# Kernel optimization log

Hardware: AMD Instinct MI355X
Metric: run time of the kernel (lower is better)

Reference implementation:

```python
import jax, jax.numpy as jnp
import numpy as np

EMB = 1024
N_HEADS = 16
HEAD = EMB // N_HEADS
EPS = 1e-5


def layernorm(x, g, b):
    mu = jnp.mean(x, axis=-1, keepdims=True)
    var = jnp.var(x, axis=-1, keepdims=True)
    return (x - mu) * jax.lax.rsqrt(var + EPS) * g + b


def setup_inputs() -> dict:
    key = jax.random.key(0)
    ks = jax.random.split(key, 12)
    s = lambda fan_in: 1.0 / np.sqrt(fan_in)
    return {
        "x": jax.random.normal(ks[0], (8, 1024, EMB), dtype=jnp.float32),
        "ln1_g": jnp.ones((EMB,), jnp.float32),
        "ln1_b": jnp.zeros((EMB,), jnp.float32),
        "wq": jax.random.uniform(ks[1], (EMB, EMB), jnp.float32, -s(EMB), s(EMB)),
        "wk": jax.random.uniform(ks[2], (EMB, EMB), jnp.float32, -s(EMB), s(EMB)),
        "wv": jax.random.uniform(ks[3], (EMB, EMB), jnp.float32, -s(EMB), s(EMB)),
        "w_proj": jax.random.uniform(ks[4], (EMB, EMB), jnp.float32, -s(EMB), s(EMB)),
        "b_proj": jnp.zeros((EMB,), jnp.float32),
        "ln2_g": jnp.ones((EMB,), jnp.float32),
        "ln2_b": jnp.zeros((EMB,), jnp.float32),
        "w1": jax.random.uniform(ks[5], (EMB, 4 * EMB), jnp.float32, -s(EMB), s(EMB)),
        "b1": jnp.zeros((4 * EMB,), jnp.float32),
        "w2": jax.random.uniform(ks[6], (4 * EMB, EMB), jnp.float32, -s(4 * EMB), s(4 * EMB)),
        "b2": jnp.zeros((EMB,), jnp.float32),
    }


def reference(x, ln1_g, ln1_b, wq, wk, wv, w_proj, b_proj, ln2_g, ln2_b, w1, b1, w2, b2):
    B, T, E = x.shape
    h = layernorm(x, ln1_g, ln1_b)
    # per-head no-bias projections == one big matmul then split into heads
    q = (h @ wq).reshape(B, T, N_HEADS, HEAD).transpose(0, 2, 1, 3)  # [B,H,T,D]
    k = (h @ wk).reshape(B, T, N_HEADS, HEAD).transpose(0, 2, 1, 3)
    v = (h @ wv).reshape(B, T, N_HEADS, HEAD).transpose(0, 2, 1, 3)
    scores = jnp.einsum("bhqd,bhkd->bhqk", q, k) * (HEAD ** -0.5)
    causal = jnp.tril(jnp.ones((T, T), dtype=bool))
    scores = jnp.where(causal, scores, -jnp.inf)
    wei = jax.nn.softmax(scores, axis=-1)  # dropout is identity at eval
    attn = jnp.einsum("bhqk,bhkd->bhqd", wei, v)
    attn = attn.transpose(0, 2, 1, 3).reshape(B, T, E)
    out = x + attn @ w_proj + b_proj
    h2 = layernorm(out, ln2_g, ln2_b)
    mlp = jax.nn.gelu(h2 @ w1 + b1, approximate=False) @ w2 + b2
    return out + mlp
```

## Files before the change

### kernel.cpp

```cpp
#include <hip/hip_runtime.h>
#include <hip/hip_bf16.h>

#define EMB 1024
#define NH 16
#define HD 64
#define BATCH 8
#define SEQ 1024
#define ROWS (BATCH*SEQ)

typedef unsigned short ushort_t;
typedef __attribute__((ext_vector_type(8))) short bf16x8;
typedef __attribute__((ext_vector_type(4))) float f32x4;

__device__ __forceinline__ float bf2f(ushort_t u){
    union { unsigned int i; float f; } v; v.i = ((unsigned int)u) << 16; return v.f;
}
__device__ __forceinline__ ushort_t f2bf(float f){
    unsigned int u = __float_as_uint(f);
    unsigned int r = (u + 0x7FFFu + ((u >> 16) & 1u)) >> 16;
    return (ushort_t)r;
}
__device__ __forceinline__ void gload16(const ushort_t* g, ushort_t* l){
    __builtin_amdgcn_global_load_lds(
        (const __attribute__((address_space(1))) void*)g,
        (__attribute__((address_space(3))) void*)l,
        16, 0, 0);
}
__device__ __forceinline__ float gelu_f(float v){
    float x = fabsf(v) * 0.70710678118654752f;
    float t = __builtin_amdgcn_rcpf(1.0f + 0.3275911f * x);
    float poly = t*(0.254829592f + t*(-0.284496736f + t*(1.421413741f + t*(-1.453152027f + t*1.061405429f))));
    float erfa = 1.0f - poly * __expf(-x*x);
    float erfv = (v >= 0.f) ? erfa : -erfa;
    return 0.5f * v * (1.0f + erfv);
}

__global__ __launch_bounds__(256) void transpose_w(const float* __restrict__ in,
                                                   ushort_t* __restrict__ out,
                                                   int K, int N){
    __shared__ ushort_t t[32][33];
    int tx = threadIdx.x & 31, ty = threadIdx.x >> 5;
    int bx = blockIdx.x, by = blockIdx.y;
    #pragma unroll
    for (int r = 0; r < 4; ++r)
        t[ty + r*8][tx] = f2bf(in[(size_t)(by*32 + ty + r*8) * N + bx*32 + tx]);
    __syncthreads();
    #pragma unroll
    for (int r = 0; r < 4; ++r)
        out[(size_t)(bx*32 + ty + r*8) * K + by*32 + tx] = t[tx][ty + r*8];
}

__global__ __launch_bounds__(256) void ln_kernel(const float* __restrict__ xin,
                                                 const float* __restrict__ g,
                                                 const float* __restrict__ bia,
                                                 ushort_t* __restrict__ out){
    int row = blockIdx.x;
    int tid = threadIdx.x;
    const float* x = xin + (size_t)row * EMB;
    float4 f = *(const float4*)(x + tid*4);
    float v[4] = {f.x, f.y, f.z, f.w};
    float s = v[0]+v[1]+v[2]+v[3];
    float q = v[0]*v[0]+v[1]*v[1]+v[2]*v[2]+v[3]*v[3];
    #pragma unroll
    for (int o = 32; o > 0; o >>= 1){ s += __shfl_down(s, o); q += __shfl_down(q, o); }
    __shared__ float ss[4], qq[4];
    __shared__ float mu_s, sc_s;
    int wave = tid >> 6, lane = tid & 63;
    if (lane == 0){ ss[wave] = s; qq[wave] = q; }
    __syncthreads();
    if (tid == 0){
        float S = ss[0]+ss[1]+ss[2]+ss[3];
        float Q = qq[0]+qq[1]+qq[2]+qq[3];
        float mu = S * (1.0f/EMB);
        float var = Q * (1.0f/EMB) - mu*mu;
        mu_s = mu; sc_s = rsqrtf(var + 1e-5f);
    }
    __syncthreads();
    float mu = mu_s, sc = sc_s;
    float4 gu = *(const float4*)(g + tid*4);
    float4 bu = *(const float4*)(bia + tid*4);
    ushort4 o4;
    o4.x = f2bf((v[0]-mu)*sc*gu.x + bu.x);
    o4.y = f2bf((v[1]-mu)*sc*gu.y + bu.y);
    o4.z = f2bf((v[2]-mu)*sc*gu.z + bu.z);
    o4.w = f2bf((v[3]-mu)*sc*gu.w + bu.w);
    *(ushort4*)(out + (size_t)row*EMB + tid*4) = o4;
}

template<int MODE>
__global__ __launch_bounds__(256) void gemm_kernel(const ushort_t* __restrict__ A,
                                                   const ushort_t* __restrict__ Bt,
                                                   const float* __restrict__ bias,
                                                   const float* __restrict__ resid,
                                                   void* __restrict__ out,
                                                   int M, int N, int K){
    __shared__ ushort_t As[128*64];
    __shared__ ushort_t Bs[128*64];
    int tid = threadIdx.x;
    int lane = tid & 63, wave = tid >> 6;
    int quad = lane >> 4, l15 = lane & 15;
    int wm = wave >> 1, wn = wave & 1;
    int m0 = blockIdx.y * 128, n0 = blockIdx.x * 128;

    f32x4 acc[4][4];
    #pragma unroll
    for (int i=0;i<4;i++)
        #pragma unroll
        for (int j=0;j<4;j++) acc[i][j] = (f32x4){0.f,0.f,0.f,0.f};

    int lr  = lane >> 3;
    int lch = lane & 7;
    const ushort_t* gA = A  + (size_t)(m0 + wave*32 + lr)*K + (lch ^ lr)*8;
    const ushort_t* gB = Bt + (size_t)(n0 + wave*32 + lr)*K + (lch ^ lr)*8;
    ushort_t* lA = &As[(wave*32)*64];
    ushort_t* lB = &Bs[(wave*32)*64];
    int sx = l15 & 7;

    for (int k0 = 0; k0 < K; k0 += 64){
        #pragma unroll
        for (int i = 0; i < 4; ++i){
            gload16(gA + (size_t)(i*8)*K + k0, lA + i*8*64);
            gload16(gB + (size_t)(i*8)*K + k0, lB + i*8*64);
        }
        __syncthreads();
        #pragma unroll
        for (int kf = 0; kf < 2; ++kf){
            int ch = (kf*4 + quad) ^ sx;
            bf16x8 af[4], bfr[4];
            #pragma unroll
            for (int i=0;i<4;i++) af[i]  = *(const bf16x8*)&As[(wm*64 + i*16 + l15)*64 + ch*8];
            #pragma unroll
            for (int j=0;j<4;j++) bfr[j] = *(const bf16x8*)&Bs[(wn*64 + j*16 + l15)*64 + ch*8];
            #pragma unroll
            for (int i=0;i<4;i++)
                #pragma unroll
                for (int j=0;j<4;j++)
                    acc[i][j] = __builtin_amdgcn_mfma_f32_16x16x32_bf16(af[i], bfr[j], acc[i][j], 0,0,0);
        }
        __syncthreads();
    }

    #pragma unroll
    for (int i=0;i<4;i++){
        int m = m0 + wm*64 + i*16 + quad*4;
        #pragma unroll
        for (int j=0;j<4;j++){
            int n = n0 + wn*64 + j*16 + l15;
            #pragma unroll
            for (int r=0;r<4;r++){
                float v = acc[i][j][r];
                size_t idx = (size_t)(m + r)*N + n;
                if (MODE == 0){
                    ((ushort_t*)out)[idx] = f2bf(v);
                } else if (MODE == 1){
                    v += bias[n] + resid[idx];
                    ((float*)out)[idx] = v;
                } else if (MODE == 2){
                    v += bias[n];
                    ((ushort_t*)out)[idx] = f2bf(gelu_f(v));
                } else {
                    v += bias[n] + resid[idx];
                    ((float*)out)[idx] = v;
                }
            }
        }
    }
}

__global__ __launch_bounds__(256) void attn_kernel(const ushort_t* __restrict__ qkv,
                                                   ushort_t* __restrict__ attn_out){
    __shared__ ushort_t Qs[128][72];
    __shared__ ushort_t Ks[64][72];
    __shared__ ushort_t Vts[64][72];
    __shared__ ushort_t Ps[128][72];

    int tid = threadIdx.x;
    int lane = tid & 63, wave = tid >> 6;
    int quad = lane >> 4, l15 = lane & 15;
    int pair = blockIdx.x;
    int bh = blockIdx.y;
    int b = bh >> 4, h = bh & 15;
    size_t tb = (size_t)b * SEQ;

    int tr = tid >> 3;
    int tc = (tid & 7) * 8;
    int sw_w = tid & 7;

    for (int t = 0; t < 2; ++t){
        int qi = t ? (7 - pair) : pair;

        #pragma unroll
        for (int p = 0; p < 4; ++p){
            int r = tr + p*32;
            size_t tok = tb + qi*128 + r;
            *(bf16x8*)&Qs[r][tc] = *(const bf16x8*)(qkv + tok*3072 + h*64 + tc);
        }

        f32x4 o_acc[2][4];
        #pragma unroll
        for (int mt=0;mt<2;mt++)
            #pragma unroll
            for (int nt=0;nt<4;nt++) o_acc[mt][nt] = (f32x4){0.f,0.f,0.f,0.f};
        float m_st[2][4], l_st[2][4];
        #pragma unroll
        for (int mt=0;mt<2;mt++)
            #pragma unroll
            for (int r=0;r<4;r++){ m_st[mt][r] = -1e30f; l_st[mt][r] = 0.f; }

        int nj = 2*qi + 2;
        for (int j = 0; j < nj; ++j){
            #pragma unroll
            for (int p = 0; p < 2; ++p){
                int r = tr + p*32;
                size_t tok = tb + j*64 + r;
                *(bf16x8*)&Ks[r][tc] = *(const bf16x8*)(qkv + tok*3072 + 1024 + h*64 + tc);
                bf16x8 vv = *(const bf16x8*)(qkv + tok*3072 + 2048 + h*64 + tc);
                int kcol = r ^ (sw_w << 3);
                #pragma unroll
                for (int c = 0; c < 8; ++c) Vts[tc + c][kcol] = (ushort_t)vv[c];
            }
            __syncthreads();

            f32x4 s_acc[2][4];
            #pragma unroll
            for (int mt=0;mt<2;mt++)
                #pragma unroll
                for (int nt=0;nt<4;nt++) s_acc[mt][nt] = (f32x4){0.f,0.f,0.f,0.f};
            #pragma unroll
            for (int kf = 0; kf < 2; ++kf){
                bf16x8 aq[2], bk[4];
                #pragma unroll
                for (int mt=0;mt<2;mt++) aq[mt] = *(const bf16x8*)&Qs[wave*32 + mt*16 + l15][kf*32 + quad*8];
                #pragma unroll
                for (int nt=0;nt<4;nt++) bk[nt] = *(const bf16x8*)&Ks[nt*16 + l15][kf*32 + quad*8];
                #pragma unroll
                for (int mt=0;mt<2;mt++)
                    #pragma unroll
                    for (int nt=0;nt<4;nt++)
                        s_acc[mt][nt] = __builtin_amdgcn_mfma_f32_16x16x32_bf16(aq[mt], bk[nt], s_acc[mt][nt], 0,0,0);
            }

            bool need_mask = (j >= 2*qi);
            #pragma unroll
            for (int mt=0;mt<2;mt++)
                #pragma unroll
                for (int nt=0;nt<4;nt++)
                    #pragma unroll
                    for (int r=0;r<4;r++){
                        float s = s_acc[mt][nt][r] * 0.125f;
                        if (need_mask){
                            int qg = qi*128 + wave*32 + mt*16 + quad*4 + r;
                            int kg = j*64 + nt*16 + l15;
                            if (kg > qg) s = -1e30f;
                        }
                        s_acc[mt][nt][r] = s;
                    }

            #pragma unroll
            for (int mt=0;mt<2;mt++){
                #pragma unroll
                for (int r=0;r<4;r++){
                    float rm = s_acc[mt][0][r];
                    #pragma unroll
                    for (int nt=1;nt<4;nt++) rm = fmaxf(rm, s_acc[mt][nt][r]);
                    rm = fmaxf(rm, __shfl_xor(rm, 1));
                    rm = fmaxf(rm, __shfl_xor(rm, 2));
                    rm = fmaxf(rm, __shfl_xor(rm, 4));
                    rm = fmaxf(rm, __shfl_xor(rm, 8));
                    float mnew = fmaxf(m_st[mt][r], rm);
                    float alpha = __expf(m_st[mt][r] - mnew);
                    float rsum = 0.f;
                    #pragma unroll
                    for (int nt=0;nt<4;nt++){
                        float p = __expf(s_acc[mt][nt][r] - mnew);
                        s_acc[mt][nt][r] = p;
                        rsum += p;
                    }
                    rsum += __shfl_xor(rsum, 1);
                    rsum += __shfl_xor(rsum, 2);
                    rsum += __shfl_xor(rsum, 4);
                    rsum += __shfl_xor(rsum, 8);
                    l_st[mt][r] = l_st[mt][r]*alpha + rsum;
                    m_st[mt][r] = mnew;
                    #pragma unroll
                    for (int nt=0;nt<4;nt++) o_acc[mt][nt][r] *= alpha;
                }
            }

            #pragma unroll
            for (int mt=0;mt<2;mt++)
                #pragma unroll
                for (int nt=0;nt<4;nt++)
                    #pragma unroll
                    for (int r=0;r<4;r++)
                        Ps[wave*32 + mt*16 + quad*4 + r][nt*16 + l15] = f2bf(s_acc[mt][nt][r]);

            #pragma unroll
            for (int kf = 0; kf < 2; ++kf){
                bf16x8 ap[2], bv[4];
                #pragma unroll
                for (int mt=0;mt<2;mt++) ap[mt] = *(const bf16x8*)&Ps[wave*32 + mt*16 + l15][kf*32 + quad*8];
                #pragma unroll
                for (int nt=0;nt<4;nt++){
                    int d = nt*16 + l15;
                    int col = (kf*32 + quad*8) ^ (((d >> 3) & 7) << 3);
                    bv[nt] = *(const bf16x8*)&Vts[d][col];
                }
                #pragma unroll
                for (int mt=0;mt<2;mt++)
                    #pragma unroll
                    for (int nt=0;nt<4;nt++)
                        o_acc[mt][nt] = __builtin_amdgcn_mfma_f32_16x16x32_bf16(ap[mt], bv[nt], o_acc[mt][nt], 0,0,0);
            }
            __syncthreads();
        }

        #pragma unroll
        for (int mt=0;mt<2;mt++)
            #pragma unroll
            for (int r=0;r<4;r++){
                float inv = 1.0f / l_st[mt][r];
                size_t tok = tb + qi*128 + wave*32 + mt*16 + quad*4 + r;
                #pragma unroll
                for (int nt=0;nt<4;nt++)
                    attn_out[tok*EMB + h*64 + nt*16 + l15] = f2bf(o_acc[mt][nt][r] * inv);
            }
    }
}

extern "C" void kernel_launch(void* const* d_in, const int* in_sizes, int n_in,
                              void* d_out, int out_size, void* d_ws, size_t ws_size,
                              hipStream_t stream){
    const float* x      = (const float*)d_in[0];
    const float* ln1_g  = (const float*)d_in[1];
    const float* ln1_b  = (const float*)d_in[2];
    const float* wq     = (const float*)d_in[3];
    const float* wk     = (const float*)d_in[4];
    const float* wv     = (const float*)d_in[5];
    const float* w_proj = (const float*)d_in[6];
    const float* b_proj = (const float*)d_in[7];
    const float* ln2_g  = (const float*)d_in[8];
    const float* ln2_b  = (const float*)d_in[9];
    const float* w1     = (const float*)d_in[10];
    const float* b1     = (const float*)d_in[11];
    const float* w2     = (const float*)d_in[12];
    const float* b2     = (const float*)d_in[13];
    float* outp = (float*)d_out;

    char* ws = (char*)d_ws;
    size_t off = 0;
    auto alloc = [&](size_t bytes)->char*{ char* p = ws + off; off += (bytes + 255) & ~255ULL; return p; };
    ushort_t* wqkv_t = (ushort_t*)alloc((size_t)3072*1024*2);
    ushort_t* wproj_t= (ushort_t*)alloc((size_t)1024*1024*2);
    ushort_t* w1_t   = (ushort_t*)alloc((size_t)4096*1024*2);
    ushort_t* w2_t   = (ushort_t*)alloc((size_t)1024*4096*2);
    ushort_t* qkv    = (ushort_t*)alloc((size_t)ROWS*3072*2);
    ushort_t* hbuf   = (ushort_t*)alloc((size_t)ROWS*1024*2);
    float*    out32  = (float*)  alloc((size_t)ROWS*1024*4);
    ushort_t* mid    = (ushort_t*)alloc((size_t)ROWS*4096*2);
    ushort_t* h1 = hbuf;
    ushort_t* attn = hbuf;
    ushort_t* h2 = qkv;

    dim3 blk(256);
    transpose_w<<<dim3(32,32),  blk, 0, stream>>>(wq,     wqkv_t,               1024, 1024);
    transpose_w<<<dim3(32,32),  blk, 0, stream>>>(wk,     wqkv_t + 1024*1024,   1024, 1024);
    transpose_w<<<dim3(32,32),  blk, 0, stream>>>(wv,     wqkv_t + 2*1024*1024, 1024, 1024);
    transpose_w<<<dim3(32,32),  blk, 0, stream>>>(w_proj, wproj_t,              1024, 1024);
    transpose_w<<<dim3(128,32), blk, 0, stream>>>(w1,     w1_t,                 1024, 4096);
    transpose_w<<<dim3(32,128), blk, 0, stream>>>(w2,     w2_t,                 4096, 1024);

    ln_kernel<<<ROWS, blk, 0, stream>>>(x, ln1_g, ln1_b, h1);
    gemm_kernel<0><<<dim3(3072/128, ROWS/128), blk, 0, stream>>>(h1, wqkv_t, nullptr, nullptr, qkv, ROWS, 3072, 1024);
    attn_kernel<<<dim3(4,128), blk, 0, stream>>>(qkv, attn);
    gemm_kernel<1><<<dim3(1024/128, ROWS/128), blk, 0, stream>>>(attn, wproj_t, b_proj, x, out32, ROWS, 1024, 1024);
    ln_kernel<<<ROWS, blk, 0, stream>>>(out32, ln2_g, ln2_b, h2);
    gemm_kernel<2><<<dim3(4096/128, ROWS/128), blk, 0, stream>>>(h2, w1_t, b1, nullptr, mid, ROWS, 4096, 1024);
    gemm_kernel<3><<<dim3(1024/128, ROWS/128), blk, 0, stream>>>(mid, w2_t, b2, out32, outp, ROWS, 1024, 4096);
}
```

Before: 541.4 us.

## Switch GEMMs to 32x32x16 MFMA and use 128x64 tiles for N=1024 GEMMs

Replaces the 16x16x32 bf16 MFMA with the 32x32x16 variant, which needs fewer LDS fragment loads per FLOP, and reworks the fragment indexing and epilogue row mapping to match. The GEMM is templated on the N tile size and the wave layout. The two N=1024 GEMMs (projection and MLP down) now use 128x64 tiles with a 4x1 wave layout, giving twice as many blocks on the 256-CU part. Smaller tiles lower data reuse per block, and the larger accumulators raise register use.

Result: no change. 546.0 us (+0.8%).

```diff
diff --git a/kernel.cpp b/kernel.cpp
--- a/kernel.cpp
+++ b/kernel.cpp
@@ -11,6 +11,7 @@
 typedef unsigned short ushort_t;
 typedef __attribute__((ext_vector_type(8))) short bf16x8;
 typedef __attribute__((ext_vector_type(4))) float f32x4;
+typedef __attribute__((ext_vector_type(16))) float f32x16;
 
 __device__ __forceinline__ float bf2f(ushort_t u){
     union { unsigned int i; float f; } v; v.i = ((unsigned int)u) << 16; return v.f;
@@ -87,69 +88,79 @@
     *(ushort4*)(out + (size_t)row*EMB + tid*4) = o4;
 }
 
-template<int MODE>
+template<int MODE, int BN, int WMW, int WNW>
 __global__ __launch_bounds__(256) void gemm_kernel(const ushort_t* __restrict__ A,
                                                    const ushort_t* __restrict__ Bt,
                                                    const float* __restrict__ bias,
                                                    const float* __restrict__ resid,
                                                    void* __restrict__ out,
                                                    int M, int N, int K){
+    constexpr int TM = 128 / WMW;
+    constexpr int TN = BN / WNW;
+    constexpr int NTM = TM / 32;
+    constexpr int NTN = TN / 32;
+    constexpr int BROWS = BN / 4;
+
     __shared__ ushort_t As[128*64];
-    __shared__ ushort_t Bs[128*64];
+    __shared__ ushort_t Bs[BN*64];
     int tid = threadIdx.x;
     int lane = tid & 63, wave = tid >> 6;
-    int quad = lane >> 4, l15 = lane & 15;
-    int wm = wave >> 1, wn = wave & 1;
-    int m0 = blockIdx.y * 128, n0 = blockIdx.x * 128;
-
-    f32x4 acc[4][4];
-    #pragma unroll
-    for (int i=0;i<4;i++)
-        #pragma unroll
-        for (int j=0;j<4;j++) acc[i][j] = (f32x4){0.f,0.f,0.f,0.f};
+    int l31 = lane & 31, half = lane >> 5;
+    int wm = wave / WNW, wn = wave % WNW;
+    int m0 = blockIdx.y * 128, n0 = blockIdx.x * BN;
+
+    f32x16 acc[NTM][NTN];
+    #pragma unroll
+    for (int i=0;i<NTM;i++)
+        #pragma unroll
+        for (int j=0;j<NTN;j++)
+            #pragma unroll
+            for (int r=0;r<16;r++) acc[i][j][r] = 0.f;
 
     int lr  = lane >> 3;
     int lch = lane & 7;
-    const ushort_t* gA = A  + (size_t)(m0 + wave*32 + lr)*K + (lch ^ lr)*8;
-    const ushort_t* gB = Bt + (size_t)(n0 + wave*32 + lr)*K + (lch ^ lr)*8;
+    const ushort_t* gA = A  + (size_t)(m0 + wave*32    + lr)*K + (lch ^ lr)*8;
+    const ushort_t* gB = Bt + (size_t)(n0 + wave*BROWS + lr)*K + (lch ^ lr)*8;
     ushort_t* lA = &As[(wave*32)*64];
-    ushort_t* lB = &Bs[(wave*32)*64];
-    int sx = l15 & 7;
+    ushort_t* lB = &Bs[(wave*BROWS)*64];
+    int sx = lane & 7;
 
     for (int k0 = 0; k0 < K; k0 += 64){
         #pragma unroll
-        for (int i = 0; i < 4; ++i){
+        for (int i = 0; i < 4; ++i)
             gload16(gA + (size_t)(i*8)*K + k0, lA + i*8*64);
+        #pragma unroll
+        for (int i = 0; i < BROWS/8; ++i)
             gload16(gB + (size_t)(i*8)*K + k0, lB + i*8*64);
-        }
         __syncthreads();
         #pragma unroll
-        for (int kf = 0; kf < 2; ++kf){
-            int ch = (kf*4 + quad) ^ sx;
-            bf16x8 af[4], bfr[4];
-            #pragma unroll
-            for (int i=0;i<4;i++) af[i]  = *(const bf16x8*)&As[(wm*64 + i*16 + l15)*64 + ch*8];
-            #pragma unroll
-            for (int j=0;j<4;j++) bfr[j] = *(const bf16x8*)&Bs[(wn*64 + j*16 + l15)*64 + ch*8];
-            #pragma unroll
-            for (int i=0;i<4;i++)
-                #pragma unroll
-                for (int j=0;j<4;j++)
-                    acc[i][j] = __builtin_amdgcn_mfma_f32_16x16x32_bf16(af[i], bfr[j], acc[i][j], 0,0,0);
+        for (int s = 0; s < 4; ++s){
+            int ch = ((s<<1) | half) ^ sx;
+            bf16x8 af[NTM], bfr[NTN];
+            #pragma unroll
+            for (int i=0;i<NTM;i++) af[i]  = *(const bf16x8*)&As[(wm*TM + i*32 + l31)*64 + ch*8];
+            #pragma unroll
+            for (int j=0;j<NTN;j++) bfr[j] = *(const bf16x8*)&Bs[(wn*TN + j*32 + l31)*64 + ch*8];
+            #pragma unroll
+            for (int i=0;i<NTM;i++)
+                #pragma unroll
+                for (int j=0;j<NTN;j++)
+                    acc[i][j] = __builtin_amdgcn_mfma_f32_32x32x16_bf16(af[i], bfr[j], acc[i][j], 0,0,0);
         }
         __syncthreads();
     }
 
-    #pragma unroll
-    for (int i=0;i<4;i++){
-        int m = m0 + wm*64 + i*16 + quad*4;
-        #pragma unroll
-        for (int j=0;j<4;j++){
-            int n = n0 + wn*64 + j*16 + l15;
-            #pragma unroll
-            for (int r=0;r<4;r++){
-                float v = acc[i][j][r];
-                size_t idx = (size_t)(m + r)*N + n;
+    int rowoff = 4*half;
+    #pragma unroll
+    for (int i=0;i<NTM;i++){
+        #pragma unroll
+        for (int j=0;j<NTN;j++){
+            int n = n0 + wn*TN + j*32 + l31;
+            #pragma unroll
+            for (int reg=0; reg<16; ++reg){
+                int m = m0 + wm*TM + i*32 + (reg&3) + 8*(reg>>2) + rowoff;
+                float v = acc[i][j][reg];
+                size_t idx = (size_t)m*N + n;
                 if (MODE == 0){
                     ((ushort_t*)out)[idx] = f2bf(v);
                 } else if (MODE == 1){
@@ -371,10 +382,10 @@
     transpose_w<<<dim3(32,128), blk, 0, stream>>>(w2,     w2_t,                 4096, 1024);
 
     ln_kernel<<<ROWS, blk, 0, stream>>>(x, ln1_g, ln1_b, h1);
-    gemm_kernel<0><<<dim3(3072/128, ROWS/128), blk, 0, stream>>>(h1, wqkv_t, nullptr, nullptr, qkv, ROWS, 3072, 1024);
+    gemm_kernel<0,128,2,2><<<dim3(3072/128, ROWS/128), blk, 0, stream>>>(h1, wqkv_t, nullptr, nullptr, qkv, ROWS, 3072, 1024);
     attn_kernel<<<dim3(4,128), blk, 0, stream>>>(qkv, attn);
-    gemm_kernel<1><<<dim3(1024/128, ROWS/128), blk, 0, stream>>>(attn, wproj_t, b_proj, x, out32, ROWS, 1024, 1024);
+    gemm_kernel<1, 64,4,1><<<dim3(1024/64,  ROWS/128), blk, 0, stream>>>(attn, wproj_t, b_proj, x, out32, ROWS, 1024, 1024);
     ln_kernel<<<ROWS, blk, 0, stream>>>(out32, ln2_g, ln2_b, h2);
-    gemm_kernel<2><<<dim3(4096/128, ROWS/128), blk, 0, stream>>>(h2, w1_t, b1, nullptr, mid, ROWS, 4096, 1024);
-    gemm_kernel<3><<<dim3(1024/128, ROWS/128), blk, 0, stream>>>(mid, w2_t, b2, out32, outp, ROWS, 1024, 4096);
-}
+    gemm_kernel<2,128,2,2><<<dim3(4096/128, ROWS/128), blk, 0, stream>>>(h2, w1_t, b1, nullptr, mid, ROWS, 4096, 1024);
+    gemm_kernel<3, 64,4,1><<<dim3(1024/64,  ROWS/128), blk, 0, stream>>>(mid, w2_t, b2, out32, outp, ROWS, 1024, 4096);
+}
```

## Use 32x32x16 MFMA tiles and M-fastest block ordering in GEMMs

Applied to the files above, without the earlier changes.

Switches the GEMM inner loop from 16x16x32 bf16 MFMAs (4x4 per wave) to 32x32x16 MFMAs (2x2 per wave), which halves LDS fragment loads per MFMA and uses the larger matrix instruction. It also flattens the grid to 1D with the M tile index varying fastest, so consecutive blocks share the same weight (B) tile for better L2 reuse. The epilogue is rewritten for the 32x32 accumulator layout, which changes store patterns and could affect coalescing.

After: 489.5 us. 1.11x faster.

```diff
diff --git a/kernel.cpp b/kernel.cpp
--- a/kernel.cpp
+++ b/kernel.cpp
@@ -7,10 +7,12 @@
 #define BATCH 8
 #define SEQ 1024
 #define ROWS (BATCH*SEQ)
+#define MT (ROWS/128)
 
 typedef unsigned short ushort_t;
 typedef __attribute__((ext_vector_type(8))) short bf16x8;
 typedef __attribute__((ext_vector_type(4))) float f32x4;
+typedef __attribute__((ext_vector_type(16))) float f32x16;
 
 __device__ __forceinline__ float bf2f(ushort_t u){
     union { unsigned int i; float f; } v; v.i = ((unsigned int)u) << 16; return v.f;
@@ -98,15 +100,18 @@
     __shared__ ushort_t Bs[128*64];
     int tid = threadIdx.x;
     int lane = tid & 63, wave = tid >> 6;
-    int quad = lane >> 4, l15 = lane & 15;
+    int l31 = lane & 31, half = lane >> 5;
     int wm = wave >> 1, wn = wave & 1;
-    int m0 = blockIdx.y * 128, n0 = blockIdx.x * 128;
-
-    f32x4 acc[4][4];
-    #pragma unroll
-    for (int i=0;i<4;i++)
-        #pragma unroll
-        for (int j=0;j<4;j++) acc[i][j] = (f32x4){0.f,0.f,0.f,0.f};
+    int bid = blockIdx.x;
+    int m0 = (bid & (MT-1)) * 128, n0 = (bid >> 6) * 128;
+
+    f32x16 acc[2][2];
+    #pragma unroll
+    for (int i=0;i<2;i++)
+        #pragma unroll
+        for (int j=0;j<2;j++)
+            #pragma unroll
+            for (int r=0;r<16;r++) acc[i][j][r] = 0.f;
 
     int lr  = lane >> 3;
     int lch = lane & 7;
@@ -114,7 +119,7 @@
     const ushort_t* gB = Bt + (size_t)(n0 + wave*32 + lr)*K + (lch ^ lr)*8;
     ushort_t* lA = &As[(wave*32)*64];
     ushort_t* lB = &Bs[(wave*32)*64];
-    int sx = l15 & 7;
+    int sx = lane & 7;
 
     for (int k0 = 0; k0 < K; k0 += 64){
         #pragma unroll
@@ -124,32 +129,33 @@
         }
         __syncthreads();
         #pragma unroll
-        for (int kf = 0; kf < 2; ++kf){
-            int ch = (kf*4 + quad) ^ sx;
-            bf16x8 af[4], bfr[4];
-            #pragma unroll
-            for (int i=0;i<4;i++) af[i]  = *(const bf16x8*)&As[(wm*64 + i*16 + l15)*64 + ch*8];
-            #pragma unroll
-            for (int j=0;j<4;j++) bfr[j] = *(const bf16x8*)&Bs[(wn*64 + j*16 + l15)*64 + ch*8];
-            #pragma unroll
-            for (int i=0;i<4;i++)
-                #pragma unroll
-                for (int j=0;j<4;j++)
-                    acc[i][j] = __builtin_amdgcn_mfma_f32_16x16x32_bf16(af[i], bfr[j], acc[i][j], 0,0,0);
+        for (int s = 0; s < 4; ++s){
+            int ch = ((s<<1) | half) ^ sx;
+            bf16x8 af[2], bfr[2];
+            #pragma unroll
+            for (int i=0;i<2;i++) af[i]  = *(const bf16x8*)&As[(wm*64 + i*32 + l31)*64 + ch*8];
+            #pragma unroll
+            for (int j=0;j<2;j++) bfr[j] = *(const bf16x8*)&Bs[(wn*64 + j*32 + l31)*64 + ch*8];
+            #pragma unroll
+            for (int i=0;i<2;i++)
+                #pragma unroll
+                for (int j=0;j<2;j++)
+                    acc[i][j] = __builtin_amdgcn_mfma_f32_32x32x16_bf16(af[i], bfr[j], acc[i][j], 0,0,0);
         }
         __syncthreads();
     }
 
-    #pragma unroll
-    for (int i=0;i<4;i++){
-        int m = m0 + wm*64 + i*16 + quad*4;
-        #pragma unroll
-        for (int j=0;j<4;j++){
-            int n = n0 + wn*64 + j*16 + l15;
-            #pragma unroll
-            for (int r=0;r<4;r++){
-                float v = acc[i][j][r];
-                size_t idx = (size_t)(m + r)*N + n;
+    int rowoff = 4*half;
+    #pragma unroll
+    for (int i=0;i<2;i++){
+        #pragma unroll
+        for (int j=0;j<2;j++){
+            int n = n0 + wn*64 + j*32 + l31;
+            #pragma unroll
+            for (int reg=0; reg<16; ++reg){
+                int m = m0 + wm*64 + i*32 + (reg&3) + 8*(reg>>2) + rowoff;
+                float v = acc[i][j][reg];
+                size_t idx = (size_t)m*N + n;
                 if (MODE == 0){
                     ((ushort_t*)out)[idx] = f2bf(v);
                 } else if (MODE == 1){
@@ -371,10 +377,10 @@
     transpose_w<<<dim3(32,128), blk, 0, stream>>>(w2,     w2_t,                 4096, 1024);
 
     ln_kernel<<<ROWS, blk, 0, stream>>>(x, ln1_g, ln1_b, h1);
-    gemm_kernel<0><<<dim3(3072/128, ROWS/128), blk, 0, stream>>>(h1, wqkv_t, nullptr, nullptr, qkv, ROWS, 3072, 1024);
+    gemm_kernel<0><<<dim3(MT*(3072/128)), blk, 0, stream>>>(h1, wqkv_t, nullptr, nullptr, qkv, ROWS, 3072, 1024);
     attn_kernel<<<dim3(4,128), blk, 0, stream>>>(qkv, attn);
-    gemm_kernel<1><<<dim3(1024/128, ROWS/128), blk, 0, stream>>>(attn, wproj_t, b_proj, x, out32, ROWS, 1024, 1024);
+    gemm_kernel<1><<<dim3(MT*(1024/128)), blk, 0, stream>>>(attn, wproj_t, b_proj, x, out32, ROWS, 1024, 1024);
     ln_kernel<<<ROWS, blk, 0, stream>>>(out32, ln2_g, ln2_b, h2);
-    gemm_kernel<2><<<dim3(4096/128, ROWS/128), blk, 0, stream>>>(h2, w1_t, b1, nullptr, mid, ROWS, 4096, 1024);
-    gemm_kernel<3><<<dim3(1024/128, ROWS/128), blk, 0, stream>>>(mid, w2_t, b2, out32, outp, ROWS, 1024, 4096);
-}
+    gemm_kernel<2><<<dim3(MT*(4096/128)), blk, 0, stream>>>(h2, w1_t, b1, nullptr, mid, ROWS, 4096, 1024);
+    gemm_kernel<3><<<dim3(MT*(1024/128)), blk, 0, stream>>>(mid, w2_t, b2, out32, outp, ROWS, 1024, 4096);
+}
```
